# Kernel optimization log

Hardware: AMD Instinct MI355X
Metric: run time of the kernel (lower is better)

The kernel has to match this reference:

```python
import jax, jax.numpy as jnp
import numpy as np

LMAX = 5
RESOLUTION = 12
ASPECT_RATIO = 2
BATCH = 256
NB = 2 * RESOLUTION                       # res_beta = 24
NA = round(2 * ASPECT_RATIO * RESOLUTION)  # res_alpha = res_gamma = 48
DIM = sum((2 * l + 1) ** 2 for l in range(LMAX + 1))  # 286

# normalize2mom constant for tanh: (E_{z~N(0,1)}[tanh(z)^2])^{-1/2}
_x = np.linspace(-12.0, 12.0, 1_000_001)
_pdf = np.exp(-0.5 * _x * _x) / np.sqrt(2.0 * np.pi)
ACT_CST = float(np.trapz(np.tanh(_x) ** 2 * _pdf, _x) ** -0.5)  # ~1.5927


def _su2_generators(j):
    m = np.arange(-j, j)
    raising = np.diag(-np.sqrt(j * (j + 1) - m * (m + 1)), k=-1).astype(complex)
    m = np.arange(-j + 1, j + 1)
    lowering = np.diag(np.sqrt(j * (j + 1) - m * (m - 1)), k=1).astype(complex)
    m = np.arange(-j, j + 1)
    return np.stack([0.5 * (raising + lowering), np.diag(1j * m), -0.5j * (raising - lowering)])


def _q_real_to_complex(l):
    q = np.zeros((2 * l + 1, 2 * l + 1), dtype=complex)
    for m in range(-l, 0):
        q[l + m, l + abs(m)] = 1 / np.sqrt(2)
        q[l + m, l - abs(m)] = -1j / np.sqrt(2)
    q[l, l] = 1
    for m in range(1, l + 1):
        q[l + m, l + abs(m)] = (-1) ** m / np.sqrt(2)
        q[l + m, l - abs(m)] = 1j * (-1) ** m / np.sqrt(2)
    return (-1j) ** l * q


def _so3_generators(l):
    X = _su2_generators(l)
    Q = _q_real_to_complex(l)
    return np.real(np.conj(Q.T)[None] @ X @ Q[None])  # real [3, 2l+1, 2l+1]


def _expm_angles(A, t):
    """exp(t_n * A) for real antisymmetric A via eigendecomposition. -> [n, d, d] real"""
    vals, vecs = np.linalg.eig(A.astype(complex))
    inv = np.linalg.inv(vecs)
    phases = np.exp(t[:, None] * vals[None, :])  # [n, d]
    return np.real(np.einsum('ij,nj,jk->nik', vecs, phases, inv))


def _build_D_and_qw():
    # Euler angle grids (e3nn SO3Grid convention)
    b = (np.arange(NB) + 0.5) / NB * np.pi          # beta   [nb]
    a = np.arange(NA) / NA * 2.0 * np.pi            # alpha=gamma [na]
    blocks = []
    for l in range(LMAX + 1):
        X = _so3_generators(l)
        Ra = _expm_angles(X[1], a)   # exp(alpha * X1)  [na,d,d]
        Rb = _expm_angles(X[0], b)   # exp(beta  * X0)  [nb,d,d]
        # D^l(a,b,c) = Ra[a] @ Rb[b] @ Ra[c]
        Dl = np.einsum('xij,yjk,zkl->xyzil', Ra, Rb, Ra)
        blocks.append(np.sqrt(2 * l + 1) * Dl.reshape(NA, NB, NA, -1))
    D = np.concatenate(blocks, axis=-1).astype(np.float32)  # [na, nb, na, dim]
    # lie_learn / Kostelec-Rockmore quadrature weights for beta
    bb = NB // 2
    k = np.arange(bb)
    j = np.arange(2 * bb)
    w = (2.0 / bb) * np.sin(np.pi * (2 * j + 1) / (4.0 * bb)) * np.sum(
        (1.0 / (2 * k + 1))[None, :]
        * np.sin((2 * j[:, None] + 1) * (2 * k[None, :] + 1) * np.pi / (4.0 * bb)),
        axis=1,
    )
    w = w / (2.0 * (2 * bb) ** 2)
    qw = (w * NB ** 2 / NA ** 2).astype(np.float32)  # [nb]
    return jnp.asarray(D), jnp.asarray(qw)


def setup_inputs() -> dict:
    key = jax.random.key(0)
    features = jax.random.normal(key, (BATCH, DIM), dtype=jnp.float32)
    D, qw = _build_D_and_qw()
    return {"features": features, "D": D, "qw": qw}


def reference(features, D, qw):
    dim = D.shape[-1]
    s = jnp.sqrt(jnp.asarray(dim, features.dtype))
    # to_grid: [B, dim] x [na, nb, na, dim] -> [B, na, nb, na]
    g = jnp.einsum('bi,xyzi->bxyz', features, D) / s
    # normalized pointwise nonlinearity on SO(3) samples
    g = ACT_CST * jnp.tanh(g)
    # from_grid: quadrature-weighted projection back onto flat Wigner basis
    return jnp.einsum('bxyz,y,xyzi->bi', g, qw, D) * s
```

## Files before the change

kernel.cpp:

```cpp
#include <hip/hip_runtime.h>
#include <hip/hip_bf16.h>

#define DIM    286
#define DIMP   288
#define NBATCH 256
#define NB_    24
#define NA_    48
#define ZC     32
#define NTILES 1728
#define NCHUNK 256
#define S_CONST 16.911534525287763f
#define INV_S   0.05913123959890826f
#define ACT_CST 1.5927f
#define TWO_LOG2E 2.8853900817779268f

typedef short bf16x8 __attribute__((ext_vector_type(8)));
typedef float f32x4  __attribute__((ext_vector_type(4)));

#define TILE_B 36864u

#define WS_FBF  0u
#define WS_DT   147456u
#define WS_PART (WS_DT + 63700992u)

typedef const __attribute__((address_space(1))) char GA;
typedef __attribute__((address_space(3))) char LA;
__device__ __forceinline__ void gload_lds16(const void* g, void* l) {
    __builtin_amdgcn_global_load_lds((GA*)g, (LA*)l, 16, 0, 0);
}

__global__ void k_prep(const float* __restrict__ F, const float* __restrict__ D,
                       const float* __restrict__ qw,
                       __hip_bfloat16* __restrict__ Fbf, char* __restrict__ DT) {
    __shared__ __align__(16) float T[9152];
    __shared__ float qs[24];
    int t = threadIdx.x;
    int bid = blockIdx.x;
    if (bid >= NTILES) {
        int o = (bid - NTILES) * 256 + t;
        int row = o / DIMP, col = o % DIMP;
        float v = (col < DIM) ? F[row * DIM + col] * INV_S : 0.f;
        Fbf[o] = __float2bfloat16(v);
        return;
    }
    int z0 = bid * 32;
    if (t < 24) qs[t] = qw[t] * S_CONST;
    {
        int wave = t >> 6, lane = t & 63;
        const char* src = (const char*)(D + (size_t)z0 * DIM);
        char* dst = (char*)T;
        #pragma unroll
        for (int j = 0; j < 9; ++j) {
            int c = wave + j * 4;
            if (c < 35 || (c == 35 && lane < 48))
                gload_lds16(src + c * 1024 + lane * 16, dst + c * 1024);
        }
    }
    asm volatile("s_waitcnt vmcnt(0)" ::: "memory");
    __syncthreads();
    char* tb = DT + (size_t)bid * TILE_B;
    for (int m = 0; m < 18; ++m) {
        int d = t + m * 256;
        int z = d / 144, i2 = d % 144;
        int i = i2 * 2;
        __hip_bfloat162 o2;
        if (i < DIM) {
            float2 v = *(const float2*)(&T[z * DIM + i]);
            o2.x = __float2bfloat16(v.x); o2.y = __float2bfloat16(v.y);
        } else {
            o2.x = __float2bfloat16(0.f); o2.y = o2.x;
        }
        int off = (((i >> 5) * 2048) + z * 64 + (i & 31) * 2) ^ ((z & 7) << 4);
        *(__hip_bfloat162*)(tb + off) = o2;
    }
    for (int s = 0; s < 5; ++s) {
        int idx = t + s * 256;
        if (idx < 1152) {
            int i = idx >> 2, zc = idx & 3;
            __hip_bfloat16 o8[8];
            #pragma unroll
            for (int j = 0; j < 8; ++j) {
                int zl = zc * 8 + j;
                int y = ((z0 + zl) / NA_) % NB_;
                o8[j] = __float2bfloat16(T[zl * DIM + i] * qs[y]);
            }
            int off = (i * 64 + zc * 16) ^ ((i & 7) << 4);
            *(bf16x8*)(tb + 18432 + off) = *(const bf16x8*)o8;
        }
    }
}

__launch_bounds__(512, 2)
__global__ void k_main(const __hip_bfloat16* __restrict__ Fbf,
                       const char* __restrict__ DT,
                       __hip_bfloat16* __restrict__ part) {
    __shared__ __align__(16) char SB[2][36864];
    __shared__ __align__(16) char GsB[16384];

    int t = threadIdx.x;
    int wave = t >> 6, lane = t & 63, ln = lane & 15, q = lane >> 4;
    int cA = (ln * 64 + q * 16) ^ ((ln & 7) << 4);

    bf16x8 fa[2][9];
    int rowbase = wave * 32;
    #pragma unroll
    for (int h = 0; h < 2; ++h) {
        const __hip_bfloat16* fp = Fbf + (size_t)(rowbase + h * 16 + ln) * DIMP + q * 8;
        #pragma unroll
        for (int ks = 0; ks < 9; ++ks) fa[h][ks] = *(const bf16x8*)(fp + ks * 32);
    }

    f32x4 acc[2][18];
    #pragma unroll
    for (int h = 0; h < 2; ++h)
        #pragma unroll
        for (int n = 0; n < 18; ++n) acc[h][n] = (f32x4){0.f, 0.f, 0.f, 0.f};

    int bx = blockIdx.x;
    int tstart = (bx < 192) ? bx * 7 : bx * 6 + 192;
    int ntile = (bx < 192) ? 7 : 6;

    const char* srcT = DT + (size_t)tstart * TILE_B;
    int lo16 = lane * 16;

    #pragma unroll
    for (int j = 0; j < 5; ++j) {
        int c = wave + j * 8;
        if (c < 36) gload_lds16(srcT + c * 1024 + lo16, SB[0] + c * 1024);
    }
    asm volatile("s_waitcnt vmcnt(0)" ::: "memory");
    __syncthreads();

    #pragma unroll 1
    for (int k = 0; k < ntile; ++k) {
        const char* cb = SB[k & 1];
        if (k + 1 < ntile) {
            const char* s2 = srcT + (size_t)(k + 1) * TILE_B;
            char* d2 = SB[(k + 1) & 1];
            #pragma unroll
            for (int j = 0; j < 5; ++j) {
                int c = wave + j * 8;
                if (c < 36) gload_lds16(s2 + c * 1024 + lo16, d2 + c * 1024);
            }
        }
        f32x4 g00 = (f32x4){0.f,0.f,0.f,0.f}, g01 = (f32x4){0.f,0.f,0.f,0.f};
        f32x4 g10 = (f32x4){0.f,0.f,0.f,0.f}, g11 = (f32x4){0.f,0.f,0.f,0.f};
        #pragma unroll
        for (int ks = 0; ks < 9; ++ks) {
            bf16x8 b0 = *(const bf16x8*)(cb + ks * 2048 + cA);
            bf16x8 b1 = *(const bf16x8*)(cb + ks * 2048 + 1024 + cA);
            g00 = __builtin_amdgcn_mfma_f32_16x16x32_bf16(fa[0][ks], b0, g00, 0, 0, 0);
            g01 = __builtin_amdgcn_mfma_f32_16x16x32_bf16(fa[0][ks], b1, g01, 0, 0, 0);
            g10 = __builtin_amdgcn_mfma_f32_16x16x32_bf16(fa[1][ks], b0, g10, 0, 0, 0);
            g11 = __builtin_amdgcn_mfma_f32_16x16x32_bf16(fa[1][ks], b1, g11, 0, 0, 0);
        }
        #pragma unroll
        for (int h = 0; h < 2; ++h) {
            #pragma unroll
            for (int zh = 0; zh < 2; ++zh) {
                f32x4 g = (h == 0) ? (zh == 0 ? g00 : g01) : (zh == 0 ? g10 : g11);
                #pragma unroll
                for (int r = 0; r < 4; ++r) {
                    float x = g[r];
                    float a = fabsf(x);
                    float e = __builtin_amdgcn_exp2f(-TWO_LOG2E * a);
                    float v = ACT_CST - 2.f * ACT_CST * e * __builtin_amdgcn_rcpf(1.f + e);
                    v = copysignf(v, x);
                    int row = h * 16 + q * 4 + r;
                    int goff = (wave << 11) + ((row * 64 + (zh * 16 + ln) * 2) ^ ((row & 7) << 4));
                    *(__hip_bfloat16*)(GsB + goff) = __float2bfloat16(v);
                }
            }
        }
        bf16x8 a20 = *(const bf16x8*)(GsB + (wave << 11) + cA);
        bf16x8 a21 = *(const bf16x8*)(GsB + (wave << 11) + 1024 + cA);
        #pragma unroll
        for (int nf = 0; nf < 18; ++nf) {
            bf16x8 b2 = *(const bf16x8*)(cb + 18432 + nf * 1024 + cA);
            acc[0][nf] = __builtin_amdgcn_mfma_f32_16x16x32_bf16(a20, b2, acc[0][nf], 0, 0, 0);
            acc[1][nf] = __builtin_amdgcn_mfma_f32_16x16x32_bf16(a21, b2, acc[1][nf], 0, 0, 0);
        }
        asm volatile("s_waitcnt vmcnt(0)" ::: "memory");
        __syncthreads();
    }
    __hip_bfloat16* pw = part + (size_t)bx * (NBATCH * DIMP) + (size_t)rowbase * DIMP;
    #pragma unroll
    for (int h = 0; h < 2; ++h) {
        #pragma unroll
        for (int m = 0; m < 9; ++m) {
            __hip_bfloat16 o8[8];
            #pragma unroll
            for (int j = 0; j < 8; ++j)
                o8[j] = __float2bfloat16(acc[h][2 * m + (j >> 2)][j & 3]);
            *(bf16x8*)(pw + (size_t)((h * 9 + m) * 64 + lane) * 8) = *(const bf16x8*)o8;
        }
    }
}

__global__ void k_reduce(const __hip_bfloat16* __restrict__ part, float* __restrict__ out) {
    __shared__ float red[3][16][8];
    int t = threadIdx.x, wave = t >> 6, lane = t & 63;
    int j = lane & 15;
    int zg = wave * 4 + (lane >> 4);
    int s = blockIdx.x * 16 + j;
    const __hip_bfloat16* p = part + (size_t)s * 8;
    float sum[8];
    #pragma unroll
    for (int kk = 0; kk < 8; ++kk) sum[kk] = 0.f;
    #pragma unroll 4
    for (int ii = 0; ii < 16; ++ii) {
        bf16x8 v = *(const bf16x8*)(p + (size_t)(zg * 16 + ii) * (NBATCH * DIMP));
        #pragma unroll
        for (int kk = 0; kk < 8; ++kk) {
            __hip_bfloat16 h; *(short*)&h = v[kk];
            sum[kk] += __bfloat162float(h);
        }
    }
    #pragma unroll
    for (int kk = 0; kk < 8; ++kk) {
        sum[kk] += __shfl_down(sum[kk], 16);
        sum[kk] += __shfl_down(sum[kk], 32);
    }
    if (wave > 0 && lane < 16) {
        #pragma unroll
        for (int kk = 0; kk < 8; ++kk) red[wave - 1][lane][kk] = sum[kk];
    }
    __syncthreads();
    if (wave == 0 && lane < 16) {
        #pragma unroll
        for (int w = 0; w < 3; ++w)
            #pragma unroll
            for (int kk = 0; kk < 8; ++kk) sum[kk] += red[w][lane][kk];
        int wr = s / 1152, si = s % 1152;
        int lane_m = si % 64, m9 = si / 64;
        int h = m9 / 9, m = m9 % 9, q = lane_m >> 4, ln = lane_m & 15;
        int rowb = wr * 32 + h * 16 + q * 4;
        #pragma unroll
        for (int j8 = 0; j8 < 8; ++j8) {
            int nf = 2 * m + (j8 >> 2), r = j8 & 3;
            int i = nf * 16 + ln;
            if (i < DIM) out[(rowb + r) * DIM + i] = sum[j8];
        }
    }
}

extern "C" void kernel_launch(void* const* d_in, const int* in_sizes, int n_in,
                              void* d_out, int out_size, void* d_ws, size_t ws_size,
                              hipStream_t stream) {
    const float* F  = (const float*)d_in[0];
    const float* D  = (const float*)d_in[1];
    const float* qw = (const float*)d_in[2];
    char* ws = (char*)d_ws;
    __hip_bfloat16* Fbf = (__hip_bfloat16*)(ws + WS_FBF);
    char* DT = ws + WS_DT;
    __hip_bfloat16* part = (__hip_bfloat16*)(ws + WS_PART);

    k_prep<<<NTILES + 288, 256, 0, stream>>>(F, D, qw, Fbf, DT);
    k_main<<<NCHUNK, 512, 0, stream>>>(Fbf, DT, part);
    k_reduce<<<576, 256, 0, stream>>>(part, (float*)d_out);
}
```

Before: 153.5 us.

## Fuse D conversion into main kernel, streaming fp32 D tiles into LDS

Removes the separate prep pass that converted D to bf16 tiles in a 64MB workspace. The main kernel now streams raw fp32 D tiles into a double-buffered LDS area with async global-to-LDS loads, converts and weights them in-kernel, then runs both GEMMs. This avoids writing and re-reading a transformed copy of D, but adds conversion work and an extra barrier per tile, and raises LDS use, which may hurt occupancy at two blocks per CU. It also changes the swizzle on the activation staging buffer.

```diff
diff --git a/kernel.cpp b/kernel.cpp
--- a/kernel.cpp
+++ b/kernel.cpp
@@ -17,11 +17,8 @@
 typedef short bf16x8 __attribute__((ext_vector_type(8)));
 typedef float f32x4  __attribute__((ext_vector_type(4)));
 
-#define TILE_B 36864u
-
 #define WS_FBF  0u
-#define WS_DT   147456u
-#define WS_PART (WS_DT + 63700992u)
+#define WS_PART 147456u
 
 typedef const __attribute__((address_space(1))) char GA;
 typedef __attribute__((address_space(3))) char LA;
@@ -29,77 +26,32 @@
     __builtin_amdgcn_global_load_lds((GA*)g, (LA*)l, 16, 0, 0);
 }
 
-__global__ void k_prep(const float* __restrict__ F, const float* __restrict__ D,
-                       const float* __restrict__ qw,
-                       __hip_bfloat16* __restrict__ Fbf, char* __restrict__ DT) {
-    __shared__ __align__(16) float T[9152];
-    __shared__ float qs[24];
-    int t = threadIdx.x;
-    int bid = blockIdx.x;
-    if (bid >= NTILES) {
-        int o = (bid - NTILES) * 256 + t;
-        int row = o / DIMP, col = o % DIMP;
-        float v = (col < DIM) ? F[row * DIM + col] * INV_S : 0.f;
-        Fbf[o] = __float2bfloat16(v);
-        return;
-    }
-    int z0 = bid * 32;
-    if (t < 24) qs[t] = qw[t] * S_CONST;
-    {
-        int wave = t >> 6, lane = t & 63;
-        const char* src = (const char*)(D + (size_t)z0 * DIM);
-        char* dst = (char*)T;
-        #pragma unroll
-        for (int j = 0; j < 9; ++j) {
-            int c = wave + j * 4;
-            if (c < 35 || (c == 35 && lane < 48))
-                gload_lds16(src + c * 1024 + lane * 16, dst + c * 1024);
-        }
-    }
-    asm volatile("s_waitcnt vmcnt(0)" ::: "memory");
-    __syncthreads();
-    char* tb = DT + (size_t)bid * TILE_B;
-    for (int m = 0; m < 18; ++m) {
-        int d = t + m * 256;
-        int z = d / 144, i2 = d % 144;
-        int i = i2 * 2;
-        __hip_bfloat162 o2;
-        if (i < DIM) {
-            float2 v = *(const float2*)(&T[z * DIM + i]);
-            o2.x = __float2bfloat16(v.x); o2.y = __float2bfloat16(v.y);
-        } else {
-            o2.x = __float2bfloat16(0.f); o2.y = o2.x;
-        }
-        int off = (((i >> 5) * 2048) + z * 64 + (i & 31) * 2) ^ ((z & 7) << 4);
-        *(__hip_bfloat162*)(tb + off) = o2;
-    }
-    for (int s = 0; s < 5; ++s) {
-        int idx = t + s * 256;
-        if (idx < 1152) {
-            int i = idx >> 2, zc = idx & 3;
-            __hip_bfloat16 o8[8];
-            #pragma unroll
-            for (int j = 0; j < 8; ++j) {
-                int zl = zc * 8 + j;
-                int y = ((z0 + zl) / NA_) % NB_;
-                o8[j] = __float2bfloat16(T[zl * DIM + i] * qs[y]);
-            }
-            int off = (i * 64 + zc * 16) ^ ((i & 7) << 4);
-            *(bf16x8*)(tb + 18432 + off) = *(const bf16x8*)o8;
-        }
-    }
+__global__ void k_prepF(const float* __restrict__ F, __hip_bfloat16* __restrict__ Fbf) {
+    int o = blockIdx.x * 256 + threadIdx.x;
+    int row = o / DIMP, col = o % DIMP;
+    float v = (col < DIM) ? F[row * DIM + col] * INV_S : 0.f;
+    Fbf[o] = __float2bfloat16(v);
 }
 
 __launch_bounds__(512, 2)
 __global__ void k_main(const __hip_bfloat16* __restrict__ Fbf,
-                       const char* __restrict__ DT,
+                       const float* __restrict__ D,
+                       const float* __restrict__ qw,
                        __hip_bfloat16* __restrict__ part) {
-    __shared__ __align__(16) char SB[2][36864];
+    __shared__ __align__(16) float Traw[2][9216];
+    __shared__ __align__(16) char DsB[18432];
+    __shared__ __align__(16) char DtB[18432];
     __shared__ __align__(16) char GsB[16384];
+    __shared__ float qs[24];
 
     int t = threadIdx.x;
     int wave = t >> 6, lane = t & 63, ln = lane & 15, q = lane >> 4;
     int cA = (ln * 64 + q * 16) ^ ((ln & 7) << 4);
+    int rq = ln * 64 + q * 16;
+    int gA0 = (wave << 11) + (rq ^ ((ln >> 2) << 4));
+    int gA1 = (wave << 11) + 1024 + (rq ^ ((4 + (ln >> 2)) << 4));
+
+    if (t < 24) qs[t] = qw[t] * S_CONST;
 
     bf16x8 fa[2][9];
     int rowbase = wave * 32;
@@ -120,35 +72,74 @@
     int tstart = (bx < 192) ? bx * 7 : bx * 6 + 192;
     int ntile = (bx < 192) ? 7 : 6;
 
-    const char* srcT = DT + (size_t)tstart * TILE_B;
-    int lo16 = lane * 16;
-
-    #pragma unroll
-    for (int j = 0; j < 5; ++j) {
-        int c = wave + j * 8;
-        if (c < 36) gload_lds16(srcT + c * 1024 + lo16, SB[0] + c * 1024);
-    }
-    asm volatile("s_waitcnt vmcnt(0)" ::: "memory");
-    __syncthreads();
+    #define STAGE(TI, BUF) do {                                                    \
+        const char* _s = (const char*)(D + (size_t)(tstart + (TI)) * 9152);        \
+        char* _d = (char*)Traw[BUF];                                               \
+        _Pragma("unroll")                                                          \
+        for (int _j = 0; _j < 5; ++_j) {                                           \
+            int _c = wave + _j * 8;                                                \
+            if (_c < 35 || (_c == 35 && lane < 48))                                \
+                gload_lds16(_s + _c * 1024 + lane * 16, _d + _c * 1024);           \
+        }                                                                          \
+    } while (0)
+
+    STAGE(0, 0);
+    STAGE(1, 1);
 
     #pragma unroll 1
     for (int k = 0; k < ntile; ++k) {
-        const char* cb = SB[k & 1];
         if (k + 1 < ntile) {
-            const char* s2 = srcT + (size_t)(k + 1) * TILE_B;
-            char* d2 = SB[(k + 1) & 1];
-            #pragma unroll
-            for (int j = 0; j < 5; ++j) {
-                int c = wave + j * 8;
-                if (c < 36) gload_lds16(s2 + c * 1024 + lo16, d2 + c * 1024);
+            if (wave < 4) asm volatile("s_waitcnt vmcnt(5)" ::: "memory");
+            else          asm volatile("s_waitcnt vmcnt(4)" ::: "memory");
+        } else {
+            asm volatile("s_waitcnt vmcnt(0)" ::: "memory");
+        }
+        __builtin_amdgcn_s_barrier();
+
+        const float* T = Traw[k & 1];
+        int z0 = (tstart + k) * 32;
+        #pragma unroll
+        for (int m = 0; m < 9; ++m) {
+            int d = t + m * 512;
+            int z = d / 144, i2 = d % 144;
+            int i = i2 * 2;
+            __hip_bfloat162 o2;
+            if (i < DIM) {
+                float2 v = *(const float2*)(&T[z * DIM + i]);
+                o2.x = __float2bfloat16(v.x); o2.y = __float2bfloat16(v.y);
+            } else {
+                o2.x = __float2bfloat16(0.f); o2.y = o2.x;
             }
-        }
+            int off = (((i >> 5) * 2048) + z * 64 + (i & 31) * 2) ^ ((z & 7) << 4);
+            *(__hip_bfloat162*)(DsB + off) = o2;
+        }
+        #pragma unroll
+        for (int s = 0; s < 3; ++s) {
+            int idx = t + s * 512;
+            if (idx < 1152) {
+                int i = idx >> 2, zc = idx & 3;
+                __hip_bfloat16 o8[8];
+                #pragma unroll
+                for (int j = 0; j < 8; ++j) {
+                    int zl = zc * 8 + j;
+                    int y = ((z0 + zl) / NA_) % NB_;
+                    o8[j] = __float2bfloat16(T[zl * DIM + i] * qs[y]);
+                }
+                int off = (i * 64 + zc * 16) ^ ((i & 7) << 4);
+                *(bf16x8*)(DtB + off) = *(const bf16x8*)o8;
+            }
+        }
+        asm volatile("s_waitcnt lgkmcnt(0)" ::: "memory");
+        __builtin_amdgcn_s_barrier();
+
+        if (k + 2 < ntile) STAGE(k + 2, k & 1);
+
         f32x4 g00 = (f32x4){0.f,0.f,0.f,0.f}, g01 = (f32x4){0.f,0.f,0.f,0.f};
         f32x4 g10 = (f32x4){0.f,0.f,0.f,0.f}, g11 = (f32x4){0.f,0.f,0.f,0.f};
         #pragma unroll
         for (int ks = 0; ks < 9; ++ks) {
-            bf16x8 b0 = *(const bf16x8*)(cb + ks * 2048 + cA);
-            bf16x8 b1 = *(const bf16x8*)(cb + ks * 2048 + 1024 + cA);
+            bf16x8 b0 = *(const bf16x8*)(DsB + ks * 2048 + cA);
+            bf16x8 b1 = *(const bf16x8*)(DsB + ks * 2048 + 1024 + cA);
             g00 = __builtin_amdgcn_mfma_f32_16x16x32_bf16(fa[0][ks], b0, g00, 0, 0, 0);
             g01 = __builtin_amdgcn_mfma_f32_16x16x32_bf16(fa[0][ks], b1, g01, 0, 0, 0);
             g10 = __builtin_amdgcn_mfma_f32_16x16x32_bf16(fa[1][ks], b0, g10, 0, 0, 0);
@@ -167,22 +158,24 @@
                     float v = ACT_CST - 2.f * ACT_CST * e * __builtin_amdgcn_rcpf(1.f + e);
                     v = copysignf(v, x);
                     int row = h * 16 + q * 4 + r;
-                    int goff = (wave << 11) + ((row * 64 + (zh * 16 + ln) * 2) ^ ((row & 7) << 4));
+                    int goff = (wave << 11)
+                             + ((row * 64 + (zh * 16 + ln) * 2) ^ ((row >> 2) << 4));
                     *(__hip_bfloat16*)(GsB + goff) = __float2bfloat16(v);
                 }
             }
         }
-        bf16x8 a20 = *(const bf16x8*)(GsB + (wave << 11) + cA);
-        bf16x8 a21 = *(const bf16x8*)(GsB + (wave << 11) + 1024 + cA);
+        bf16x8 a20 = *(const bf16x8*)(GsB + gA0);
+        bf16x8 a21 = *(const bf16x8*)(GsB + gA1);
         #pragma unroll
         for (int nf = 0; nf < 18; ++nf) {
-            bf16x8 b2 = *(const bf16x8*)(cb + 18432 + nf * 1024 + cA);
+            bf16x8 b2 = *(const bf16x8*)(DtB + nf * 1024 + cA);
             acc[0][nf] = __builtin_amdgcn_mfma_f32_16x16x32_bf16(a20, b2, acc[0][nf], 0, 0, 0);
             acc[1][nf] = __builtin_amdgcn_mfma_f32_16x16x32_bf16(a21, b2, acc[1][nf], 0, 0, 0);
         }
-        asm volatile("s_waitcnt vmcnt(0)" ::: "memory");
-        __syncthreads();
-    }
+        __builtin_amdgcn_s_barrier();
+    }
+    #undef STAGE
+
     __hip_bfloat16* pw = part + (size_t)bx * (NBATCH * DIMP) + (size_t)rowbase * DIMP;
     #pragma unroll
     for (int h = 0; h < 2; ++h) {
@@ -252,10 +245,9 @@
     const float* qw = (const float*)d_in[2];
     char* ws = (char*)d_ws;
     __hip_bfloat16* Fbf = (__hip_bfloat16*)(ws + WS_FBF);
-    char* DT = ws + WS_DT;
     __hip_bfloat16* part = (__hip_bfloat16*)(ws + WS_PART);
 
-    k_prep<<<NTILES + 288, 256, 0, stream>>>(F, D, qw, Fbf, DT);
-    k_main<<<NCHUNK, 512, 0, stream>>>(Fbf, DT, part);
+    k_prepF<<<288, 256, 0, stream>>>(F, Fbf);
+    k_main<<<NCHUNK, 512, 0, stream>>>(Fbf, D, qw, part);
     k_reduce<<<576, 256, 0, stream>>>(part, (float*)d_out);
 }
```

Result: slower. 206.9 us (+34.8%).

## Split batch across two 256-thread blocks, single-buffer D tiles, stream features from global

Applied to the files above, without the earlier changes.

k_main now launches a 2D grid in which each 256-thread block handles 128 batch rows instead of one 512-thread block handling all 256. LDS drops to a single D-tile buffer plus a smaller G buffer, and the feature A-operands are reloaded from global memory inside the k-loop rather than held in registers. The aim is lower LDS and register pressure so more blocks fit per CU, with occupancy standing in for the old explicit double-buffering. The cost is that every D tile is now loaded twice (once per batch half), the load is no longer overlapped with compute within a block, and the repeated global feature loads add latency; the G swizzle also changes.

```diff
diff --git a/kernel.cpp b/kernel.cpp
--- a/kernel.cpp
+++ b/kernel.cpp
@@ -90,25 +90,23 @@
     }
 }
 
-__launch_bounds__(512, 2)
+__launch_bounds__(256, 2)
 __global__ void k_main(const __hip_bfloat16* __restrict__ Fbf,
                        const char* __restrict__ DT,
                        __hip_bfloat16* __restrict__ part) {
-    __shared__ __align__(16) char SB[2][36864];
-    __shared__ __align__(16) char GsB[16384];
+    __shared__ __align__(16) char SB[36864];
+    __shared__ __align__(16) char GsB[8192];
 
     int t = threadIdx.x;
     int wave = t >> 6, lane = t & 63, ln = lane & 15, q = lane >> 4;
     int cA = (ln * 64 + q * 16) ^ ((ln & 7) << 4);
-
-    bf16x8 fa[2][9];
-    int rowbase = wave * 32;
-    #pragma unroll
-    for (int h = 0; h < 2; ++h) {
-        const __hip_bfloat16* fp = Fbf + (size_t)(rowbase + h * 16 + ln) * DIMP + q * 8;
-        #pragma unroll
-        for (int ks = 0; ks < 9; ++ks) fa[h][ks] = *(const bf16x8*)(fp + ks * 32);
-    }
+    int rq = ln * 64 + q * 16;
+    int gA0 = (wave << 11) + (rq ^ ((ln >> 2) << 4));
+    int gA1 = (wave << 11) + 1024 + (rq ^ ((4 + (ln >> 2)) << 4));
+
+    int rowbase = blockIdx.y * 128 + wave * 32;
+    const __hip_bfloat16* fp0 = Fbf + (size_t)(rowbase + ln) * DIMP + q * 8;
+    const __hip_bfloat16* fp1 = fp0 + 16 * DIMP;
 
     f32x4 acc[2][18];
     #pragma unroll
@@ -120,39 +118,30 @@
     int tstart = (bx < 192) ? bx * 7 : bx * 6 + 192;
     int ntile = (bx < 192) ? 7 : 6;
 
-    const char* srcT = DT + (size_t)tstart * TILE_B;
-    int lo16 = lane * 16;
-
-    #pragma unroll
-    for (int j = 0; j < 5; ++j) {
-        int c = wave + j * 8;
-        if (c < 36) gload_lds16(srcT + c * 1024 + lo16, SB[0] + c * 1024);
-    }
-    asm volatile("s_waitcnt vmcnt(0)" ::: "memory");
-    __syncthreads();
-
     #pragma unroll 1
     for (int k = 0; k < ntile; ++k) {
-        const char* cb = SB[k & 1];
-        if (k + 1 < ntile) {
-            const char* s2 = srcT + (size_t)(k + 1) * TILE_B;
-            char* d2 = SB[(k + 1) & 1];
-            #pragma unroll
-            for (int j = 0; j < 5; ++j) {
-                int c = wave + j * 8;
-                if (c < 36) gload_lds16(s2 + c * 1024 + lo16, d2 + c * 1024);
-            }
-        }
+        {
+            const char* src = DT + (size_t)(tstart + k) * TILE_B + wave * 9216 + lane * 16;
+            char* dst = SB + wave * 9216;
+            #pragma unroll
+            for (int j = 0; j < 9; ++j)
+                gload_lds16(src + j * 1024, dst + j * 1024);
+        }
+        asm volatile("s_waitcnt vmcnt(0)" ::: "memory");
+        __syncthreads();
+
         f32x4 g00 = (f32x4){0.f,0.f,0.f,0.f}, g01 = (f32x4){0.f,0.f,0.f,0.f};
         f32x4 g10 = (f32x4){0.f,0.f,0.f,0.f}, g11 = (f32x4){0.f,0.f,0.f,0.f};
-        #pragma unroll
+        #pragma unroll 3
         for (int ks = 0; ks < 9; ++ks) {
-            bf16x8 b0 = *(const bf16x8*)(cb + ks * 2048 + cA);
-            bf16x8 b1 = *(const bf16x8*)(cb + ks * 2048 + 1024 + cA);
-            g00 = __builtin_amdgcn_mfma_f32_16x16x32_bf16(fa[0][ks], b0, g00, 0, 0, 0);
-            g01 = __builtin_amdgcn_mfma_f32_16x16x32_bf16(fa[0][ks], b1, g01, 0, 0, 0);
-            g10 = __builtin_amdgcn_mfma_f32_16x16x32_bf16(fa[1][ks], b0, g10, 0, 0, 0);
-            g11 = __builtin_amdgcn_mfma_f32_16x16x32_bf16(fa[1][ks], b1, g11, 0, 0, 0);
+            bf16x8 a0 = *(const bf16x8*)(fp0 + ks * 32);
+            bf16x8 a1 = *(const bf16x8*)(fp1 + ks * 32);
+            bf16x8 b0 = *(const bf16x8*)(SB + ks * 2048 + cA);
+            bf16x8 b1 = *(const bf16x8*)(SB + ks * 2048 + 1024 + cA);
+            g00 = __builtin_amdgcn_mfma_f32_16x16x32_bf16(a0, b0, g00, 0, 0, 0);
+            g01 = __builtin_amdgcn_mfma_f32_16x16x32_bf16(a0, b1, g01, 0, 0, 0);
+            g10 = __builtin_amdgcn_mfma_f32_16x16x32_bf16(a1, b0, g10, 0, 0, 0);
+            g11 = __builtin_amdgcn_mfma_f32_16x16x32_bf16(a1, b1, g11, 0, 0, 0);
         }
         #pragma unroll
         for (int h = 0; h < 2; ++h) {
@@ -167,22 +156,23 @@
                     float v = ACT_CST - 2.f * ACT_CST * e * __builtin_amdgcn_rcpf(1.f + e);
                     v = copysignf(v, x);
                     int row = h * 16 + q * 4 + r;
-                    int goff = (wave << 11) + ((row * 64 + (zh * 16 + ln) * 2) ^ ((row & 7) << 4));
+                    int goff = (wave << 11)
+                             + ((row * 64 + (zh * 16 + ln) * 2) ^ ((row >> 2) << 4));
                     *(__hip_bfloat16*)(GsB + goff) = __float2bfloat16(v);
                 }
             }
         }
-        bf16x8 a20 = *(const bf16x8*)(GsB + (wave << 11) + cA);
-        bf16x8 a21 = *(const bf16x8*)(GsB + (wave << 11) + 1024 + cA);
+        bf16x8 a20 = *(const bf16x8*)(GsB + gA0);
+        bf16x8 a21 = *(const bf16x8*)(GsB + gA1);
         #pragma unroll
         for (int nf = 0; nf < 18; ++nf) {
-            bf16x8 b2 = *(const bf16x8*)(cb + 18432 + nf * 1024 + cA);
+            bf16x8 b2 = *(const bf16x8*)(SB + 18432 + nf * 1024 + cA);
             acc[0][nf] = __builtin_amdgcn_mfma_f32_16x16x32_bf16(a20, b2, acc[0][nf], 0, 0, 0);
             acc[1][nf] = __builtin_amdgcn_mfma_f32_16x16x32_bf16(a21, b2, acc[1][nf], 0, 0, 0);
         }
-        asm volatile("s_waitcnt vmcnt(0)" ::: "memory");
         __syncthreads();
     }
+
     __hip_bfloat16* pw = part + (size_t)bx * (NBATCH * DIMP) + (size_t)rowbase * DIMP;
     #pragma unroll
     for (int h = 0; h < 2; ++h) {
@@ -256,6 +246,6 @@
     __hip_bfloat16* part = (__hip_bfloat16*)(ws + WS_PART);
 
     k_prep<<<NTILES + 288, 256, 0, stream>>>(F, D, qw, Fbf, DT);
-    k_main<<<NCHUNK, 512, 0, stream>>>(Fbf, DT, part);
+    k_main<<<dim3(NCHUNK, 2), 256, 0, stream>>>(Fbf, DT, part);
     k_reduce<<<576, 256, 0, stream>>>(part, (float*)d_out);
 }
```

Result: faster. 150.1 us (-2.2%).
